# Optimization experiments

Measured on AMD Instinct MI355X. Metric: run time of the kernel, lower is better.

Reference implementation:

```python
import jax, jax.numpy as jnp
import numpy as np
from jax import lax

T, B, D, H, O = 256, 128, 1024, 1024, 1024


def setup_inputs() -> dict:
    key = jax.random.key(0)
    ks = jax.random.split(key, 12)
    s_in = 1.0 / np.sqrt(D + H)  # torch Linear default init scale (approx)
    s_h = 1.0 / np.sqrt(H)
    return {
        "x": jax.random.normal(ks[0], (T, B, D), jnp.float32),
        "Wf": jax.random.normal(ks[1], (H, D + H), jnp.float32) * s_in,
        "bf": jax.random.normal(ks[2], (H,), jnp.float32) * s_in,
        "Wi": jax.random.normal(ks[3], (H, D + H), jnp.float32) * s_in,
        "bi": jax.random.normal(ks[4], (H,), jnp.float32) * s_in,
        "Wg": jax.random.normal(ks[5], (H, D + H), jnp.float32) * s_in,
        "bg": jax.random.normal(ks[6], (H,), jnp.float32) * s_in,
        "Wo": jax.random.normal(ks[7], (H, D + H), jnp.float32) * s_in,
        "bo": jax.random.normal(ks[8], (H,), jnp.float32) * s_in,
        "Wout": jax.random.normal(ks[9], (O, H), jnp.float32) * s_h,
        "bout": jax.random.normal(ks[10], (H,), jnp.float32) * s_h,
    }


def reference(x, Wf, bf, Wi, bi, Wg, bg, Wo, bo, Wout, bout):
    # x: [T, B, D] time-major. Single-layer LSTM (num_layers=1 collapses state).
    # Fuse the 4 gate GEMMs into one: W4 [4H, D+H]
    W4 = jnp.concatenate([Wf, Wi, Wg, Wo], axis=0)
    b4 = jnp.concatenate([bf, bi, bg, bo], axis=0)
    Hh = Wf.shape[0]
    h0 = jnp.zeros((x.shape[1], Hh), x.dtype)
    c0 = jnp.zeros((x.shape[1], Hh), x.dtype)

    def step(carry, xt):
        h, c = carry
        s = jnp.concatenate([xt, h], axis=-1)  # [B, D+H]
        z = s @ W4.T + b4                       # [B, 4H]
        zi, zf, zg, zo = jnp.split(z, 4, axis=-1)
        # note: original code applies forget_gate weights to i_t and
        # input_gate weights to f_t (naming swap); math preserved.
        i_t = jax.nn.sigmoid(zi)
        f_t = jax.nn.sigmoid(zf)
        g_t = jnp.tanh(zg)
        o_t = jax.nn.sigmoid(zo)
        c = f_t * c + i_t * g_t
        h = o_t * jnp.tanh(c)
        return (h, c), None

    (hT, _), _ = lax.scan(step, (h0, c0), x)
    logits = hT @ Wout.T + bout  # [B, O]
    return jax.nn.log_softmax(logits, axis=-1)
```

## Files before the change

kernel.cpp:

```cpp
#include <hip/hip_runtime.h>

typedef __bf16 bf16;
typedef __bf16 bf16x8 __attribute__((ext_vector_type(8)));
typedef float f32x4 __attribute__((ext_vector_type(4)));
typedef unsigned int u32x4 __attribute__((ext_vector_type(4)));

#define T_STEPS 256
#define NWG 256

__device__ __forceinline__ float fast_sigmoid(float v) {
    return __fdividef(1.0f, 1.0f + __expf(-v));
}
__device__ __forceinline__ float fast_tanh(float v) {
    v = fminf(fmaxf(v, -15.0f), 15.0f);
    float e2 = __expf(2.0f * v);
    return __fdividef(e2 - 1.0f, e2 + 1.0f);
}

__global__ void init_kernel(const float* __restrict__ x, bf16* __restrict__ xb,
                            bf16* __restrict__ hb0, unsigned int* __restrict__ flags) {
    int gid = blockIdx.x * blockDim.x + threadIdx.x;
    {
        const float* src = x + (size_t)gid * 8;
        float4 v0 = *(const float4*)(src);
        float4 v1 = *(const float4*)(src + 4);
        bf16x8 f;
        f[0]=(bf16)v0.x; f[1]=(bf16)v0.y; f[2]=(bf16)v0.z; f[3]=(bf16)v0.w;
        f[4]=(bf16)v1.x; f[5]=(bf16)v1.y; f[6]=(bf16)v1.z; f[7]=(bf16)v1.w;
        *(bf16x8*)(xb + (size_t)gid * 8) = f;
    }
    if (gid < 16384) *(u32x4*)(hb0 + gid * 8) = (u32x4){0u, 0u, 0u, 0u};
    if (gid < 4096)  flags[gid] = 0u;
}

__global__ __launch_bounds__(512, 2) void lstm_persist(
    const bf16* __restrict__ xb,
    const float* __restrict__ Wf, const float* __restrict__ bfp,
    const float* __restrict__ Wi, const float* __restrict__ bip,
    const float* __restrict__ Wg, const float* __restrict__ bgp,
    const float* __restrict__ Wo, const float* __restrict__ bop,
    bf16* __restrict__ hb, unsigned int* __restrict__ flags)
{
    __shared__ bf16 S[4 * 32 * 264];
    __shared__ float zb[8 * 2112];

    const int wg   = blockIdx.x;
    const int mq   = wg & 3;
    const int tile = wg >> 2;
    const int tid  = threadIdx.x;
    const int lane = tid & 63;
    const int w    = tid >> 6;
    const int l16  = lane & 15;
    const int l4   = lane >> 4;

    const float* Wptr[4] = {Wf, Wi, Wg, Wo};
    bf16x8 bfrag[4][8];
    #pragma unroll
    for (int g = 0; g < 4; ++g) {
        const float* wrow = Wptr[g] + (size_t)(tile * 16 + l16) * 2048 + 256 * w + l4 * 8;
        #pragma unroll
        for (int ks = 0; ks < 8; ++ks) {
            float4 a = *(const float4*)(wrow + ks * 32);
            float4 b = *(const float4*)(wrow + ks * 32 + 4);
            bf16x8 f;
            f[0]=(bf16)a.x; f[1]=(bf16)a.y; f[2]=(bf16)a.z; f[3]=(bf16)a.w;
            f[4]=(bf16)b.x; f[5]=(bf16)b.y; f[6]=(bf16)b.z; f[7]=(bf16)b.w;
            bfrag[g][ks] = f;
        }
    }

    const int cb = tid >> 3;
    const int cp = tid & 7;
    float bias0[2], bias1[2], bias2[2], bias3[2];
    if (tid < 256) {
        #pragma unroll
        for (int j = 0; j < 2; ++j) {
            int col = tile * 16 + 2 * cp + j;
            bias0[j] = bfp[col];
            bias1[j] = bip[col];
            bias2[j] = bgp[col];
            bias3[j] = bop[col];
        }
    }
    float creg0 = 0.0f, creg1 = 0.0f;

    for (int t = 0; t < T_STEPS; ++t) {
        f32x4 acc[2][4];
        #pragma unroll
        for (int mt = 0; mt < 2; ++mt)
            #pragma unroll
            for (int g = 0; g < 4; ++g) acc[mt][g] = (f32x4){0.f, 0.f, 0.f, 0.f};

        if (w < 4) {
            const bf16* xrow = xb + (size_t)t * 131072 + (size_t)(mq * 32 + l16) * 1024
                               + 256 * w + l4 * 8;
            #pragma unroll
            for (int half = 0; half < 2; ++half) {
                bf16x8 af[4][2];
                #pragma unroll
                for (int ks = 0; ks < 4; ++ks)
                    #pragma unroll
                    for (int mt = 0; mt < 2; ++mt)
                        af[ks][mt] = *(const bf16x8*)(xrow + (half * 4 + ks) * 32
                                                      + (size_t)mt * 16 * 1024);
                #pragma unroll
                for (int ks = 0; ks < 4; ++ks)
                    #pragma unroll
                    for (int mt = 0; mt < 2; ++mt)
                        #pragma unroll
                        for (int g = 0; g < 4; ++g)
                            acc[mt][g] = __builtin_amdgcn_mfma_f32_16x16x32_bf16(
                                af[ks][mt], bfrag[g][half * 4 + ks], acc[mt][g], 0, 0, 0);
            }
        } else {
            const int hw = w - 4;
            bf16* Sw = S + hw * 32 * 264;
            if (t > 0) {
                const unsigned int* fl = flags + (mq * 64 + lane) * 16;
                unsigned int fv;
                do {
                    fv = __hip_atomic_load(fl, __ATOMIC_RELAXED, __HIP_MEMORY_SCOPE_SYSTEM);
                } while (__any((int)(fv < (unsigned int)t)));
            }
            const bf16* hcur = hb + (t & 1) * 131072;
            #pragma unroll
            for (int half = 0; half < 2; ++half) {
                u32x4 tmp[8];
                #pragma unroll
                for (int i = 0; i < 8; ++i) {
                    int linear = half * 512 + i * 64 + lane;
                    int row = linear >> 5, chunk = linear & 31;
                    const void* g = hcur + (size_t)(mq * 32 + row) * 1024 + hw * 256 + chunk * 8;
                    asm volatile("global_load_dwordx4 %0, %1, off sc0 sc1"
                                 : "=v"(tmp[i]) : "v"(g));
                }
                asm volatile("s_waitcnt vmcnt(0)" ::: "memory");
                #pragma unroll
                for (int i = 0; i < 8; ++i) {
                    int linear = half * 512 + i * 64 + lane;
                    int row = linear >> 5, chunk = linear & 31;
                    *(u32x4*)(&Sw[row * 264 + chunk * 8]) = tmp[i];
                }
            }
            #pragma unroll
            for (int ks = 0; ks < 8; ++ks) {
                bf16x8 af[2];
                #pragma unroll
                for (int mt = 0; mt < 2; ++mt)
                    af[mt] = *(const bf16x8*)(&Sw[(mt * 16 + l16) * 264 + (ks * 4 + l4) * 8]);
                #pragma unroll
                for (int mt = 0; mt < 2; ++mt)
                    #pragma unroll
                    for (int g = 0; g < 4; ++g)
                        acc[mt][g] = __builtin_amdgcn_mfma_f32_16x16x32_bf16(
                            af[mt], bfrag[g][ks], acc[mt][g], 0, 0, 0);
            }
        }

        {
            float* pb = zb + w * 2112;
            #pragma unroll
            for (int mt = 0; mt < 2; ++mt)
                #pragma unroll
                for (int g = 0; g < 4; ++g)
                    #pragma unroll
                    for (int r = 0; r < 4; ++r)
                        pb[(mt * 16 + l4 * 4 + r) * 66 + g * 16 + l16] = acc[mt][g][r];
        }
        __syncthreads();

        if (tid < 256) {
            float z[4][2];
            #pragma unroll
            for (int g = 0; g < 4; ++g) {
                z[g][0] = 0.f; z[g][1] = 0.f;
            }
            #pragma unroll
            for (int k = 0; k < 8; ++k) {
                const float* pb = zb + k * 2112 + cb * 66;
                #pragma unroll
                for (int g = 0; g < 4; ++g) {
                    float2 v = *(const float2*)(pb + g * 16 + 2 * cp);
                    z[g][0] += v.x; z[g][1] += v.y;
                }
            }
            float hv[2];
            #pragma unroll
            for (int j = 0; j < 2; ++j) {
                float ig = fast_sigmoid(z[0][j] + bias0[j]);
                float fg = fast_sigmoid(z[1][j] + bias1[j]);
                float gg = fast_tanh   (z[2][j] + bias2[j]);
                float og = fast_sigmoid(z[3][j] + bias3[j]);
                float& cr = j ? creg1 : creg0;
                cr = fg * cr + ig * gg;
                hv[j] = og * fast_tanh(cr);
            }
            unsigned short u0 = __builtin_bit_cast(unsigned short, (bf16)hv[0]);
            unsigned short u1 = __builtin_bit_cast(unsigned short, (bf16)hv[1]);
            unsigned int packed = ((unsigned int)u1 << 16) | u0;
            unsigned int* dst = (unsigned int*)(hb + ((t + 1) & 1) * 131072
                                + (size_t)(mq * 32 + cb) * 1024 + tile * 16 + 2 * cp);
            __hip_atomic_store(dst, packed, __ATOMIC_RELAXED, __HIP_MEMORY_SCOPE_SYSTEM);
            asm volatile("s_waitcnt vmcnt(0)" ::: "memory");
        }
        __syncthreads();
        if (tid == 0)
            __hip_atomic_store(flags + (mq * 64 + tile) * 16, (unsigned int)(t + 1),
                               __ATOMIC_RELAXED, __HIP_MEMORY_SCOPE_SYSTEM);
    }
}

__global__ __launch_bounds__(512) void final_gemm_kernel(
    const bf16* __restrict__ hfin, const float* __restrict__ Wout,
    const float* __restrict__ bout, float* __restrict__ logits) {
    __shared__ alignas(16) bf16 Slds[128 * 72];
    const int tid  = threadIdx.x;
    const int lane = tid & 63;
    const int wave = tid >> 6;
    const int l16  = lane & 15;
    const int l4   = lane >> 4;
    const int n0   = blockIdx.x * 16;
    f32x4 acc = (f32x4){0.f, 0.f, 0.f, 0.f};
    for (int k0 = 0; k0 < 1024; k0 += 64) {
        #pragma unroll
        for (int i = 0; i < 2; ++i) {
            int cidx = tid + i * 512;
            int row = cidx >> 3, c8 = cidx & 7;
            *(uint4*)(&Slds[row * 72 + c8 * 8]) =
                *(const uint4*)(hfin + row * 1024 + k0 + c8 * 8);
        }
        __syncthreads();
        #pragma unroll
        for (int kk = 0; kk < 64; kk += 32) {
            const float* wrow = Wout + (size_t)(n0 + l16) * 1024 + k0 + kk + l4 * 8;
            float4 w0 = *(const float4*)(wrow);
            float4 w1 = *(const float4*)(wrow + 4);
            bf16x8 bfrag;
            bfrag[0]=(bf16)w0.x; bfrag[1]=(bf16)w0.y; bfrag[2]=(bf16)w0.z; bfrag[3]=(bf16)w0.w;
            bfrag[4]=(bf16)w1.x; bfrag[5]=(bf16)w1.y; bfrag[6]=(bf16)w1.z; bfrag[7]=(bf16)w1.w;
            bf16x8 afrag = *(const bf16x8*)(&Slds[(wave * 16 + l16) * 72 + kk + l4 * 8]);
            acc = __builtin_amdgcn_mfma_f32_16x16x32_bf16(afrag, bfrag, acc, 0, 0, 0);
        }
        __syncthreads();
    }
    float bv = bout[n0 + l16];
    #pragma unroll
    for (int r = 0; r < 4; ++r) {
        int m = wave * 16 + l4 * 4 + r;
        logits[m * 1024 + n0 + l16] = acc[r] + bv;
    }
}

__global__ __launch_bounds__(256) void logsoftmax_kernel(
    const float* __restrict__ logits, float* __restrict__ out) {
    int b = blockIdx.x, tid = threadIdx.x;
    int lane = tid & 63, wv = tid >> 6;
    __shared__ float red[4];
    float v[4];
    float mx = -1e30f;
    #pragma unroll
    for (int i = 0; i < 4; ++i) {
        v[i] = logits[b * 1024 + i * 256 + tid];
        mx = fmaxf(mx, v[i]);
    }
    #pragma unroll
    for (int off = 1; off < 64; off <<= 1) mx = fmaxf(mx, __shfl_xor(mx, off));
    if (lane == 0) red[wv] = mx;
    __syncthreads();
    mx = fmaxf(fmaxf(red[0], red[1]), fmaxf(red[2], red[3]));
    float s = 0.f;
    #pragma unroll
    for (int i = 0; i < 4; ++i) s += __expf(v[i] - mx);
    #pragma unroll
    for (int off = 1; off < 64; off <<= 1) s += __shfl_xor(s, off);
    __syncthreads();
    if (lane == 0) red[wv] = s;
    __syncthreads();
    s = red[0] + red[1] + red[2] + red[3];
    float lse = mx + __logf(s);
    #pragma unroll
    for (int i = 0; i < 4; ++i) out[b * 1024 + i * 256 + tid] = v[i] - lse;
}

extern "C" void kernel_launch(void* const* d_in, const int* in_sizes, int n_in,
                              void* d_out, int out_size, void* d_ws, size_t ws_size,
                              hipStream_t stream) {
    const float* x    = (const float*)d_in[0];
    const float* Wf   = (const float*)d_in[1];
    const float* bfv  = (const float*)d_in[2];
    const float* Wi   = (const float*)d_in[3];
    const float* biv  = (const float*)d_in[4];
    const float* Wg   = (const float*)d_in[5];
    const float* bgv  = (const float*)d_in[6];
    const float* Wo   = (const float*)d_in[7];
    const float* bov  = (const float*)d_in[8];
    const float* Wout = (const float*)d_in[9];
    const float* bout = (const float*)d_in[10];
    float* out = (float*)d_out;

    char* p = (char*)d_ws;
    bf16* xb      = (bf16*)p;  p += (size_t)T_STEPS * 131072 * 2;
    bf16* hbuf    = (bf16*)p;  p += (size_t)2 * 131072 * 2;
    float* logits = (float*)p; p += (size_t)131072 * 4;
    unsigned int* flags = (unsigned int*)p; p += 4096 * 4;
    if (ws_size < (size_t)(p - (char*)d_ws)) return;

    init_kernel<<<16384, 256, 0, stream>>>(x, xb, hbuf, flags);
    lstm_persist<<<NWG, 512, 0, stream>>>(xb, Wf, bfv, Wi, biv, Wg, bgv, Wo, bov,
                                          hbuf, flags);
    final_gemm_kernel<<<64, 512, 0, stream>>>(hbuf, Wout, bout, logits);
    logsoftmax_kernel<<<128, 256, 0, stream>>>(logits, out);
}
```

Before: 1.514 ms.

## Load h straight into MFMA registers, use per-wave flags, double-buffer partial sums

The recurrent h operand is now loaded from global memory directly into registers in the MFMA fragment layout, skipping the LDS staging copy. Each consumer lane polls its own fine-grained flag, and each producer wave publishes its own flag right after storing, instead of one flag per workgroup behind a block barrier. The gate partial-sum buffer is double-buffered by step parity so the trailing __syncthreads can be dropped. The aim is to shorten the per-step critical path of the serial recurrence, at the cost of more flag traffic and more registers held for the loaded h values.

After: 1.981 ms. 1.31x slower.

```diff
diff --git a/kernel.cpp b/kernel.cpp
--- a/kernel.cpp
+++ b/kernel.cpp
@@ -41,8 +41,7 @@
     const float* __restrict__ Wo, const float* __restrict__ bop,
     bf16* __restrict__ hb, unsigned int* __restrict__ flags)
 {
-    __shared__ bf16 S[4 * 32 * 264];
-    __shared__ float zb[8 * 2112];
+    __shared__ float zb[2][8][2112];
 
     const int wg   = blockIdx.x;
     const int mq   = wg & 3;
@@ -85,6 +84,7 @@
     float creg0 = 0.0f, creg1 = 0.0f;
 
     for (int t = 0; t < T_STEPS; ++t) {
+        const int p = t & 1;
         f32x4 acc[2][4];
         #pragma unroll
         for (int mt = 0; mt < 2; ++mt)
@@ -114,51 +114,48 @@
             }
         } else {
             const int hw = w - 4;
-            bf16* Sw = S + hw * 32 * 264;
             if (t > 0) {
-                const unsigned int* fl = flags + (mq * 64 + lane) * 16;
+                const unsigned int* fl = flags + (size_t)(mq * 256 + hw * 64 + lane) * 4;
                 unsigned int fv;
                 do {
                     fv = __hip_atomic_load(fl, __ATOMIC_RELAXED, __HIP_MEMORY_SCOPE_SYSTEM);
-                } while (__any((int)(fv < (unsigned int)t)));
-            }
-            const bf16* hcur = hb + (t & 1) * 131072;
-            #pragma unroll
-            for (int half = 0; half < 2; ++half) {
-                u32x4 tmp[8];
-                #pragma unroll
-                for (int i = 0; i < 8; ++i) {
-                    int linear = half * 512 + i * 64 + lane;
-                    int row = linear >> 5, chunk = linear & 31;
-                    const void* g = hcur + (size_t)(mq * 32 + row) * 1024 + hw * 256 + chunk * 8;
-                    asm volatile("global_load_dwordx4 %0, %1, off sc0 sc1"
-                                 : "=v"(tmp[i]) : "v"(g));
-                }
-                asm volatile("s_waitcnt vmcnt(0)" ::: "memory");
-                #pragma unroll
-                for (int i = 0; i < 8; ++i) {
-                    int linear = half * 512 + i * 64 + lane;
-                    int row = linear >> 5, chunk = linear & 31;
-                    *(u32x4*)(&Sw[row * 264 + chunk * 8]) = tmp[i];
-                }
-            }
+                } while (fv < (unsigned int)t);
+            }
+            const bf16* hbase = hb + p * 131072 + (size_t)(mq * 32 + l16) * 1024
+                                + hw * 256 + l4 * 8;
+            u32x4 hv0[8], hv1[8];
+            #pragma unroll
+            for (int ks = 0; ks < 8; ++ks)
+                asm volatile("global_load_dwordx4 %0, %1, off sc0 sc1"
+                             : "=v"(hv0[ks]) : "v"((const void*)(hbase + ks * 32)));
+            #pragma unroll
+            for (int ks = 0; ks < 8; ++ks)
+                asm volatile("global_load_dwordx4 %0, %1, off sc0 sc1"
+                             : "=v"(hv1[ks]) : "v"((const void*)(hbase + 16 * 1024 + ks * 32)));
+            asm volatile("s_waitcnt vmcnt(8)" ::: "memory");
+            __builtin_amdgcn_sched_barrier(0);
             #pragma unroll
             for (int ks = 0; ks < 8; ++ks) {
-                bf16x8 af[2];
-                #pragma unroll
-                for (int mt = 0; mt < 2; ++mt)
-                    af[mt] = *(const bf16x8*)(&Sw[(mt * 16 + l16) * 264 + (ks * 4 + l4) * 8]);
-                #pragma unroll
-                for (int mt = 0; mt < 2; ++mt)
-                    #pragma unroll
-                    for (int g = 0; g < 4; ++g)
-                        acc[mt][g] = __builtin_amdgcn_mfma_f32_16x16x32_bf16(
-                            af[mt], bfrag[g][ks], acc[mt][g], 0, 0, 0);
+                bf16x8 a = __builtin_bit_cast(bf16x8, hv0[ks]);
+                #pragma unroll
+                for (int g = 0; g < 4; ++g)
+                    acc[0][g] = __builtin_amdgcn_mfma_f32_16x16x32_bf16(
+                        a, bfrag[g][ks], acc[0][g], 0, 0, 0);
+            }
+            asm volatile("s_waitcnt vmcnt(0)" ::: "memory");
+            __builtin_amdgcn_sched_barrier(0);
+            #pragma unroll
+            for (int ks = 0; ks < 8; ++ks) {
+                bf16x8 a = __builtin_bit_cast(bf16x8, hv1[ks]);
+                #pragma unroll
+                for (int g = 0; g < 4; ++g)
+                    acc[1][g] = __builtin_amdgcn_mfma_f32_16x16x32_bf16(
+                        a, bfrag[g][ks], acc[1][g], 0, 0, 0);
             }
         }
 
         {
-            float* pb = zb + w * 2112;
+            float* pb = &zb[p][w][0];
             #pragma unroll
             for (int mt = 0; mt < 2; ++mt)
                 #pragma unroll
@@ -177,7 +174,7 @@
             }
             #pragma unroll
             for (int k = 0; k < 8; ++k) {
-                const float* pb = zb + k * 2112 + cb * 66;
+                const float* pb = &zb[p][k][cb * 66];
                 #pragma unroll
                 for (int g = 0; g < 4; ++g) {
                     float2 v = *(const float2*)(pb + g * 16 + 2 * cp);
@@ -202,11 +199,11 @@
                                 + (size_t)(mq * 32 + cb) * 1024 + tile * 16 + 2 * cp);
             __hip_atomic_store(dst, packed, __ATOMIC_RELAXED, __HIP_MEMORY_SCOPE_SYSTEM);
             asm volatile("s_waitcnt vmcnt(0)" ::: "memory");
-        }
-        __syncthreads();
-        if (tid == 0)
-            __hip_atomic_store(flags + (mq * 64 + tile) * 16, (unsigned int)(t + 1),
-                               __ATOMIC_RELAXED, __HIP_MEMORY_SCOPE_SYSTEM);
+            if (lane == 0)
+                __hip_atomic_store(flags + (size_t)(mq * 256 + tile * 4 + w) * 4,
+                                   (unsigned int)(t + 1),
+                                   __ATOMIC_RELAXED, __HIP_MEMORY_SCOPE_SYSTEM);
+        }
     }
 }
 
```
